# Kernel optimization log

Hardware: AMD Instinct MI355X
Metric: run time of the kernel (lower is better)

Reference implementation:

```python
import jax, jax.numpy as jnp
import numpy as np

B, N, D_IN, D_OUT, H = 8, 1024, 768, 768, 12
D_HEAD = D_OUT // H  # 64; per-head softmax scale is sqrt(D_HEAD)


def setup_inputs() -> dict:
    key = jax.random.key(0)
    kx, kq, kk, kv, kwo, kbo = jax.random.split(key, 6)
    s_in = 1.0 / np.sqrt(D_IN)
    s_out = 1.0 / np.sqrt(D_OUT)
    return {
        "x": jax.random.normal(kx, (B, N, D_IN), dtype=jnp.float32),
        # stacked per-head Linear weights, torch layout [out, in] -> [H, d_head, D_IN]
        "Wq": jax.random.uniform(kq, (H, D_HEAD, D_IN), jnp.float32, -s_in, s_in),
        "Wk": jax.random.uniform(kk, (H, D_HEAD, D_IN), jnp.float32, -s_in, s_in),
        "Wv": jax.random.uniform(kv, (H, D_HEAD, D_IN), jnp.float32, -s_in, s_in),
        "Wo": jax.random.uniform(kwo, (D_OUT, D_OUT), jnp.float32, -s_out, s_out),
        "bo": jax.random.uniform(kbo, (D_OUT,), jnp.float32, -s_out, s_out),
    }


def reference(x, Wq, Wk, Wv, Wo, bo):
    # Per-head projections, batched over heads: [B, H, N, d_head]
    q = jnp.einsum('bnd,hed->bhne', x, Wq)
    k = jnp.einsum('bnd,hed->bhne', x, Wk)
    v = jnp.einsum('bnd,hed->bhne', x, Wv)
    scale = 1.0 / np.sqrt(D_HEAD)
    scores = jnp.einsum('bhie,bhje->bhij', q, k) * scale  # [B, H, N, N]
    att = jax.nn.softmax(scores, axis=-1)
    out = jnp.einsum('bhij,bhje->bhie', att, v)  # [B, H, N, d_head]
    # concat heads along last dim: [B, N, H*d_head]
    out = out.transpose(0, 2, 1, 3).reshape(B, N, D_OUT)
    return out @ Wo.T + bo
```

## Files before the change

### kernel.cpp

```cpp
#include <hip/hip_runtime.h>
#include <hip/hip_bf16.h>


typedef unsigned short u16;
typedef unsigned int u32;
typedef __attribute__((ext_vector_type(8))) short bf8;
typedef __attribute__((ext_vector_type(4))) short bf4;
typedef __attribute__((ext_vector_type(4))) float f4;
typedef __attribute__((ext_vector_type(4))) unsigned short us4;

#define NB 8
#define NSEQ 1024
#define DMODEL 768
#define NHEAD 12
#define DHEAD 64

#define XELEMS   (NB * NSEQ * DMODEL)
#define WELEMS   (DMODEL * DMODEL)

__device__ __forceinline__ float b2f(u16 u) {
  union { unsigned int i; float f; } c; c.i = ((unsigned int)u) << 16; return c.f;
}
__device__ __forceinline__ u16 f2b(float f) {
  union { float f; unsigned int i; } c; c.f = f;
  unsigned int r = c.i + 0x7fffu + ((c.i >> 16) & 1u);
  return (u16)(r >> 16);
}
__device__ __forceinline__ void gl_lds16(const u16* g, u16* l) {
  __builtin_amdgcn_global_load_lds(
      (const __attribute__((address_space(1))) unsigned int*)g,
      (__attribute__((address_space(3))) unsigned int*)l, 16, 0, 0);
}

struct CvtArgs {
  const float* src[5];
  u16* dst[5];
};
#define G0 (XELEMS / 4)
#define GW (WELEMS / 4)
#define GTOT (G0 + 4 * GW)

__global__ __launch_bounds__(256) void cvt_kernel(CvtArgs a) {
  size_t g = (size_t)blockIdx.x * 256 + threadIdx.x;
  if (g >= GTOT) return;
  int t; size_t off;
  if (g < G0) { t = 0; off = g; }
  else { size_t r = g - G0; t = 1 + (int)(r / GW); off = r % GW; }
  f4 v = *(const f4*)(a.src[t] + off * 4);
  us4 o;
  o[0] = f2b(v[0]); o[1] = f2b(v[1]); o[2] = f2b(v[2]); o[3] = f2b(v[3]);
  *(us4*)(a.dst[t] + off * 4) = o;
}

__global__ __launch_bounds__(256, 2) void qkv_gemm(
    const u16* __restrict__ x, const u16* __restrict__ Wq,
    const u16* __restrict__ Wk, const u16* __restrict__ Wv,
    u16* __restrict__ q, u16* __restrict__ k, u16* __restrict__ vt)
{
  __shared__ __align__(16) u16 lA[2][128 * 64];
  __shared__ __align__(16) u16 lB[2][128 * 64];

  const int tid  = threadIdx.x;
  const int lane = tid & 63;
  const int w    = tid >> 6;
  const int wm   = w >> 1;
  const int wn   = w & 1;
  const int col  = lane & 15;
  const int quad = lane >> 4;

  const int bid = blockIdx.x;
  const int xcd = bid & 7;
  const int j   = bid >> 3;
  const int bng = j / 48;
  const int rr  = j % 48;
  const int bm8 = rr / 6;
  const int bn6 = rr % 6;
  const int bm  = xcd * 8 + bm8;
  const int bn  = bng * 6 + bn6;

  const int m0 = bm * 128;
  const int proj = bn / 6;
  const u16* Wsel = (proj == 0) ? Wq : (proj == 1 ? Wk : Wv);
  const int nrem0 = (bn % 6) * 128;

  const int srow8 = lane >> 3;
  const int sg    = (lane & 7) ^ srow8;

  const u16* gA = x    + (size_t)(m0    + w * 32 + srow8) * DMODEL + sg * 8;
  const u16* gB = Wsel + (size_t)(nrem0 + w * 32 + srow8) * DMODEL + sg * 8;

  f4 acc[4][4];
#pragma unroll
  for (int i = 0; i < 4; i++)
#pragma unroll
    for (int jj = 0; jj < 4; jj++) acc[i][jj] = (f4)0.0f;

#define QKV_STAGE(T, BUF)                                                      \
  do {                                                                         \
    const int kk_ = (T) * 64;                                                  \
    _Pragma("unroll")                                                          \
    for (int i_ = 0; i_ < 4; i_++)                                             \
      gl_lds16(gA + (size_t)(i_ * 8) * DMODEL + kk_,                           \
               &lA[BUF][(w * 32 + i_ * 8) * 64]);                              \
    _Pragma("unroll")                                                          \
    for (int i_ = 0; i_ < 4; i_++)                                             \
      gl_lds16(gB + (size_t)(i_ * 8) * DMODEL + kk_,                           \
               &lB[BUF][(w * 32 + i_ * 8) * 64]);                              \
  } while (0)

  QKV_STAGE(0, 0);
  __syncthreads();

  for (int t = 0; t < 12; t++) {
    const int cur = t & 1;
    if (t < 11) QKV_STAGE(t + 1, cur ^ 1);

    bf8 af[4][2], bfr[4][2];
#pragma unroll
    for (int mt = 0; mt < 4; mt++) {
      const int row = wm * 64 + mt * 16 + col;
#pragma unroll
      for (int kt = 0; kt < 2; kt++)
        af[mt][kt] = *(const bf8*)&lA[cur][row * 64 + (((kt * 4 + quad) ^ (row & 7)) << 3)];
    }
#pragma unroll
    for (int nt = 0; nt < 4; nt++) {
      const int row = wn * 64 + nt * 16 + col;
#pragma unroll
      for (int kt = 0; kt < 2; kt++)
        bfr[nt][kt] = *(const bf8*)&lB[cur][row * 64 + (((kt * 4 + quad) ^ (row & 7)) << 3)];
    }

    __builtin_amdgcn_s_setprio(1);
#pragma unroll
    for (int mt = 0; mt < 4; mt++)
#pragma unroll
      for (int nt = 0; nt < 4; nt++)
#pragma unroll
        for (int kt = 0; kt < 2; kt++)
          acc[mt][nt] = __builtin_amdgcn_mfma_f32_16x16x32_bf16(af[mt][kt], bfr[nt][kt], acc[mt][nt], 0, 0, 0);
    __builtin_amdgcn_s_setprio(0);

    __syncthreads();
  }
#undef QKV_STAGE

  const int mw0 = m0 + wm * 64, nw0 = nrem0 + wn * 64;
  if (proj == 2) {
#pragma unroll
    for (int mt = 0; mt < 4; mt++) {
#pragma unroll
      for (int nt = 0; nt < 4; nt++) {
        const int nc = nw0 + nt * 16 + col;
        const int h = nc >> 6, e = nc & 63;
        const int t0 = mw0 + mt * 16 + quad * 4;
        const int b = t0 >> 10, tok0 = t0 & 1023;
        us4 pk;
#pragma unroll
        for (int r = 0; r < 4; r++) pk[r] = f2b(acc[mt][nt][r]);
        *(us4*)(vt + ((size_t)(b * NHEAD + h) * DHEAD + e) * NSEQ + tok0) = pk;
      }
    }
  } else {
    u16* dst = (proj == 0) ? q : k;
#pragma unroll
    for (int mt = 0; mt < 4; mt++) {
#pragma unroll
      for (int nt = 0; nt < 4; nt++) {
        const int nc = nw0 + nt * 16 + col;
        const int h = nc >> 6, e = nc & 63;
#pragma unroll
        for (int r = 0; r < 4; r++) {
          const int t = mw0 + mt * 16 + quad * 4 + r;
          const int b = t >> 10, tok = t & 1023;
          dst[((size_t)(b * NHEAD + h) * NSEQ + tok) * DHEAD + e] = f2b(acc[mt][nt][r]);
        }
      }
    }
  }
}

__global__ __launch_bounds__(256, 3) void attn_kernel(
    const u16* __restrict__ q, const u16* __restrict__ k,
    const u16* __restrict__ vt, u16* __restrict__ attn)
{
  __shared__ __align__(16) u16 ldsK[2][64 * 64];
  __shared__ __align__(16) u16 ldsV[2][64 * 64];
  __shared__ __align__(16) u16 ldsP[4][32][72];

  const int tid  = threadIdx.x;
  const int lane = tid & 63;
  const int w    = tid >> 6;
  const int col  = lane & 15;
  const int quad = lane >> 4;

  const int idx = blockIdx.x;
  const int bh = idx % 96, qc = idx / 96;
  const int b = bh / 12, h = bh % 12;

  const size_t head = ((size_t)b * NHEAD + h) * NSEQ * DHEAD;
  const int q0 = qc * 128 + w * 32;

  const int srow8 = lane >> 3;
  const int sg    = (lane & 7) ^ srow8;

  bf8 onesf;
#pragma unroll
  for (int jj = 0; jj < 8; jj++) onesf[jj] = (short)0x3F80;

  bf8 qf[2][2];
#pragma unroll
  for (int qt = 0; qt < 2; qt++)
#pragma unroll
    for (int kt = 0; kt < 2; kt++) {
      const int row = q0 + qt * 16 + col;
      bf8 t = *(const bf8*)(q + head + (size_t)row * DHEAD + kt * 32 + quad * 8);
#pragma unroll
      for (int jj = 0; jj < 8; jj++) t[jj] = (short)f2b(b2f((u16)t[jj]) * 0.125f);
      qf[qt][kt] = t;
    }

  f4 lacc[2];
  f4 o[2][4];
#pragma unroll
  for (int mt = 0; mt < 2; mt++) {
    lacc[mt] = (f4)0.0f;
#pragma unroll
    for (int et = 0; et < 4; et++) o[mt][et] = (f4)0.0f;
  }

#pragma unroll
  for (int i = 0; i < 2; i++) {
    const int li = w * 2 + i;
    gl_lds16(k  + head + (size_t)(li * 8 + srow8) * DHEAD + sg * 8, &ldsK[0][li * 512]);
    gl_lds16(vt + head + (size_t)(li * 8 + srow8) * NSEQ + sg * 8,  &ldsV[0][li * 512]);
  }

  for (int t = 0; t < NSEQ / 64; t++) {
    const int cur = t & 1;
    __syncthreads();
    if (t < NSEQ / 64 - 1) {
      const int kb2 = (t + 1) * 64;
#pragma unroll
      for (int i = 0; i < 2; i++) {
        const int li = w * 2 + i;
        gl_lds16(k  + head + (size_t)(kb2 + li * 8 + srow8) * DHEAD + sg * 8,
                 &ldsK[cur ^ 1][li * 512]);
        gl_lds16(vt + head + (size_t)(li * 8 + srow8) * NSEQ + kb2 + sg * 8,
                 &ldsV[cur ^ 1][li * 512]);
      }
    }

    f4 st[4][2];
#pragma unroll
    for (int kvt = 0; kvt < 4; kvt++)
#pragma unroll
      for (int qt = 0; qt < 2; qt++) st[kvt][qt] = (f4)0.0f;
#pragma unroll
    for (int kt = 0; kt < 2; kt++) {
      bf8 kf[4];
#pragma unroll
      for (int kvt = 0; kvt < 4; kvt++) {
        const int row = kvt * 16 + col;
        kf[kvt] = *(const bf8*)&ldsK[cur][row * 64 + (((kt * 4 + quad) ^ (col & 7)) << 3)];
      }
      __builtin_amdgcn_s_setprio(1);
#pragma unroll
      for (int kvt = 0; kvt < 4; kvt++)
#pragma unroll
        for (int qt = 0; qt < 2; qt++)
          st[kvt][qt] = __builtin_amdgcn_mfma_f32_16x16x32_bf16(kf[kvt], qf[qt][kt], st[kvt][qt], 0, 0, 0);
      __builtin_amdgcn_s_setprio(0);
    }

#pragma unroll
    for (int kvt = 0; kvt < 4; kvt++)
#pragma unroll
      for (int qt = 0; qt < 2; qt++) {
        const f4 p = st[kvt][qt];
        bf4 pw;
        pw[0] = (short)f2b(__expf(p[0]));
        pw[1] = (short)f2b(__expf(p[1]));
        pw[2] = (short)f2b(__expf(p[2]));
        pw[3] = (short)f2b(__expf(p[3]));
        *(bf4*)&ldsP[w][qt * 16 + col][kvt * 16 + quad * 4] = pw;
      }
    asm volatile("" ::: "memory");

#pragma unroll
    for (int kt2 = 0; kt2 < 2; kt2++) {
      bf8 vf[4];
#pragma unroll
      for (int et = 0; et < 4; et++) {
        const int row = et * 16 + col;
        vf[et] = *(const bf8*)&ldsV[cur][row * 64 + (((kt2 * 4 + quad) ^ (col & 7)) << 3)];
      }
#pragma unroll
      for (int mt = 0; mt < 2; mt++) {
        const bf8 pf = *(const bf8*)&ldsP[w][mt * 16 + col][kt2 * 32 + quad * 8];
        __builtin_amdgcn_s_setprio(1);
        lacc[mt] = __builtin_amdgcn_mfma_f32_16x16x32_bf16(pf, onesf, lacc[mt], 0, 0, 0);
#pragma unroll
        for (int et = 0; et < 4; et++)
          o[mt][et] = __builtin_amdgcn_mfma_f32_16x16x32_bf16(pf, vf[et], o[mt][et], 0, 0, 0);
        __builtin_amdgcn_s_setprio(0);
      }
    }
  }

#pragma unroll
  for (int mt = 0; mt < 2; mt++)
#pragma unroll
    for (int r = 0; r < 4; r++) {
      const float inv = 1.0f / lacc[mt][r];
      const int token = q0 + mt * 16 + quad * 4 + r;
#pragma unroll
      for (int et = 0; et < 4; et++)
        attn[(size_t)(b * NSEQ + token) * DMODEL + h * DHEAD + et * 16 + col] =
            f2b(o[mt][et][r] * inv);
    }
}

__global__ __launch_bounds__(256, 4) void out_gemm(
    const u16* __restrict__ attn, const u16* __restrict__ Wo,
    const float* __restrict__ bo, float* __restrict__ out)
{
  __shared__ __align__(16) u16 lA[2][128 * 32];
  __shared__ __align__(16) u16 lB[2][128 * 32];

  const int tid  = threadIdx.x;
  const int lane = tid & 63;
  const int w    = tid >> 6;
  const int wm   = w >> 1, wn = w & 1;
  const int col  = lane & 15;
  const int quad = lane >> 4;
  const int bm = blockIdx.x;
  const int bn = blockIdx.y;

  const int m0 = bm * 128;
  const int n0 = bn * 128;

  const int srow = lane >> 2;
  const int sg   = (lane & 3) ^ ((srow >> 1) & 3);
  const u16* gA0 = attn + (size_t)(m0 + w * 32 + srow) * DMODEL + sg * 8;
  const u16* gB0 = Wo   + (size_t)(n0 + w * 32 + srow) * DMODEL + sg * 8;

  f4 acc[4][4];
#pragma unroll
  for (int i = 0; i < 4; i++)
#pragma unroll
    for (int jj = 0; jj < 4; jj++) acc[i][jj] = (f4)0.0f;

  gl_lds16(gA0, &lA[0][(w * 32) * 32]);
  gl_lds16(gA0 + (size_t)16 * DMODEL, &lA[0][(w * 32 + 16) * 32]);
  gl_lds16(gB0, &lB[0][(w * 32) * 32]);
  gl_lds16(gB0 + (size_t)16 * DMODEL, &lB[0][(w * 32 + 16) * 32]);

  for (int it = 0; it < 24; it++) {
    const int cur = it & 1;
    __syncthreads();
    if (it < 23) {
      const int kk = (it + 1) * 32;
      gl_lds16(gA0 + kk, &lA[cur ^ 1][(w * 32) * 32]);
      gl_lds16(gA0 + (size_t)16 * DMODEL + kk, &lA[cur ^ 1][(w * 32 + 16) * 32]);
      gl_lds16(gB0 + kk, &lB[cur ^ 1][(w * 32) * 32]);
      gl_lds16(gB0 + (size_t)16 * DMODEL + kk, &lB[cur ^ 1][(w * 32 + 16) * 32]);
    }

    bf8 af[4], bfr[4];
#pragma unroll
    for (int mt = 0; mt < 4; mt++) {
      const int row = wm * 64 + mt * 16 + col;
      af[mt] = *(const bf8*)&lA[cur][row * 32 + ((quad ^ ((row >> 1) & 3)) << 3)];
    }
#pragma unroll
    for (int nt = 0; nt < 4; nt++) {
      const int row = wn * 64 + nt * 16 + col;
      bfr[nt] = *(const bf8*)&lB[cur][row * 32 + ((quad ^ ((row >> 1) & 3)) << 3)];
    }
#pragma unroll
    for (int mt = 0; mt < 4; mt++)
#pragma unroll
      for (int nt = 0; nt < 4; nt++)
        acc[mt][nt] = __builtin_amdgcn_mfma_f32_16x16x32_bf16(af[mt], bfr[nt], acc[mt][nt], 0, 0, 0);
  }

  const int mw0 = m0 + wm * 64, nw0 = n0 + wn * 64;
#pragma unroll
  for (int mt = 0; mt < 4; mt++)
#pragma unroll
    for (int nt = 0; nt < 4; nt++) {
      const int n = nw0 + nt * 16 + col;
      const float bias = bo[n];
#pragma unroll
      for (int r = 0; r < 4; r++) {
        const int row = mw0 + mt * 16 + quad * 4 + r;
        out[(size_t)row * DMODEL + n] = acc[mt][nt][r] + bias;
      }
    }
}

extern "C" void kernel_launch(void* const* d_in, const int* in_sizes, int n_in,
                              void* d_out, int out_size, void* d_ws, size_t ws_size,
                              hipStream_t stream) {
  const float* x  = (const float*)d_in[0];
  const float* Wq = (const float*)d_in[1];
  const float* Wk = (const float*)d_in[2];
  const float* Wv = (const float*)d_in[3];
  const float* Wo = (const float*)d_in[4];
  const float* bo = (const float*)d_in[5];
  float* out = (float*)d_out;

  u16* xb   = (u16*)d_ws;
  u16* wqb  = xb  + XELEMS;
  u16* wkb  = wqb + WELEMS;
  u16* wvb  = wkb + WELEMS;
  u16* wob  = wvb + WELEMS;
  u16* q    = wob + WELEMS;
  u16* k    = q   + XELEMS;
  u16* vt   = k   + XELEMS;
  u16* attn = vt  + XELEMS;

  CvtArgs ca;
  ca.src[0] = x;  ca.src[1] = Wq;  ca.src[2] = Wk;  ca.src[3] = Wv;  ca.src[4] = Wo;
  ca.dst[0] = xb; ca.dst[1] = wqb; ca.dst[2] = wkb; ca.dst[3] = wvb; ca.dst[4] = wob;

  cvt_kernel<<<dim3((GTOT + 255) / 256), 256, 0, stream>>>(ca);
  qkv_gemm<<<dim3(1152), 256, 0, stream>>>(xb, wqb, wkb, wvb, q, k, vt);
  attn_kernel<<<dim3(768), 256, 0, stream>>>(q, k, vt, attn);
  out_gemm<<<dim3(64, 6), 256, 0, stream>>>(attn, wob, bo, out);
}
```

Measured before the change: 185.8 us.

## Fold query scale into QKV epilogue and deepen output GEMM K-tile with XCD swizzle

The 1/sqrt(d_head) scale now multiplies Q in the QKV projection epilogue, so the attention kernel no longer converts and rescales its Q fragments. The output projection GEMM doubles its K tile to 64 with an 8-way XOR swizzle, halving the loop trips and barriers. Its grid becomes 1D with an XCD-aware block remap for L2 locality, and the MFMA block gets raised priority. The larger LDS footprint lowers the occupancy hint from 4 to 2 blocks per CU.

```diff
diff --git a/kernel.cpp b/kernel.cpp
--- a/kernel.cpp
+++ b/kernel.cpp
@@ -163,6 +163,7 @@
     }
   } else {
     u16* dst = (proj == 0) ? q : k;
+    const float scl = (proj == 0) ? 0.125f : 1.0f;
 #pragma unroll
     for (int mt = 0; mt < 4; mt++) {
 #pragma unroll
@@ -173,7 +174,7 @@
         for (int r = 0; r < 4; r++) {
           const int t = mw0 + mt * 16 + quad * 4 + r;
           const int b = t >> 10, tok = t & 1023;
-          dst[((size_t)(b * NHEAD + h) * NSEQ + tok) * DHEAD + e] = f2b(acc[mt][nt][r]);
+          dst[((size_t)(b * NHEAD + h) * NSEQ + tok) * DHEAD + e] = f2b(acc[mt][nt][r] * scl);
         }
       }
     }
@@ -214,10 +215,7 @@
 #pragma unroll
     for (int kt = 0; kt < 2; kt++) {
       const int row = q0 + qt * 16 + col;
-      bf8 t = *(const bf8*)(q + head + (size_t)row * DHEAD + kt * 32 + quad * 8);
-#pragma unroll
-      for (int jj = 0; jj < 8; jj++) t[jj] = (short)f2b(b2f((u16)t[jj]) * 0.125f);
-      qf[qt][kt] = t;
+      qf[qt][kt] = *(const bf8*)(q + head + (size_t)row * DHEAD + kt * 32 + quad * 8);
     }
 
   f4 lacc[2];
@@ -321,29 +319,35 @@
     }
 }
 
-__global__ __launch_bounds__(256, 4) void out_gemm(
+__global__ __launch_bounds__(256, 2) void out_gemm(
     const u16* __restrict__ attn, const u16* __restrict__ Wo,
     const float* __restrict__ bo, float* __restrict__ out)
 {
-  __shared__ __align__(16) u16 lA[2][128 * 32];
-  __shared__ __align__(16) u16 lB[2][128 * 32];
+  __shared__ __align__(16) u16 lA[2][128 * 64];
+  __shared__ __align__(16) u16 lB[2][128 * 64];
 
   const int tid  = threadIdx.x;
   const int lane = tid & 63;
   const int w    = tid >> 6;
-  const int wm   = w >> 1, wn = w & 1;
+  const int wm   = w >> 1;
+  const int wn   = w & 1;
   const int col  = lane & 15;
   const int quad = lane >> 4;
-  const int bm = blockIdx.x;
-  const int bn = blockIdx.y;
+
+  const int bid = blockIdx.x;
+  const int xcd = bid & 7;
+  const int j   = bid >> 3;
+  const int bm  = xcd * 8 + j / 6;
+  const int bn  = j % 6;
 
   const int m0 = bm * 128;
   const int n0 = bn * 128;
 
-  const int srow = lane >> 2;
-  const int sg   = (lane & 3) ^ ((srow >> 1) & 3);
-  const u16* gA0 = attn + (size_t)(m0 + w * 32 + srow) * DMODEL + sg * 8;
-  const u16* gB0 = Wo   + (size_t)(n0 + w * 32 + srow) * DMODEL + sg * 8;
+  const int srow8 = lane >> 3;
+  const int sg    = (lane & 7) ^ srow8;
+
+  const u16* gA = attn + (size_t)(m0 + w * 32 + srow8) * DMODEL + sg * 8;
+  const u16* gB = Wo   + (size_t)(n0 + w * 32 + srow8) * DMODEL + sg * 8;
 
   f4 acc[4][4];
 #pragma unroll
@@ -351,39 +355,55 @@
 #pragma unroll
     for (int jj = 0; jj < 4; jj++) acc[i][jj] = (f4)0.0f;
 
-  gl_lds16(gA0, &lA[0][(w * 32) * 32]);
-  gl_lds16(gA0 + (size_t)16 * DMODEL, &lA[0][(w * 32 + 16) * 32]);
-  gl_lds16(gB0, &lB[0][(w * 32) * 32]);
-  gl_lds16(gB0 + (size_t)16 * DMODEL, &lB[0][(w * 32 + 16) * 32]);
-
-  for (int it = 0; it < 24; it++) {
-    const int cur = it & 1;
-    __syncthreads();
-    if (it < 23) {
-      const int kk = (it + 1) * 32;
-      gl_lds16(gA0 + kk, &lA[cur ^ 1][(w * 32) * 32]);
-      gl_lds16(gA0 + (size_t)16 * DMODEL + kk, &lA[cur ^ 1][(w * 32 + 16) * 32]);
-      gl_lds16(gB0 + kk, &lB[cur ^ 1][(w * 32) * 32]);
-      gl_lds16(gB0 + (size_t)16 * DMODEL + kk, &lB[cur ^ 1][(w * 32 + 16) * 32]);
-    }
-
-    bf8 af[4], bfr[4];
+#define OUT_STAGE(T, BUF)                                                      \
+  do {                                                                         \
+    const int kk_ = (T) * 64;                                                  \
+    _Pragma("unroll")                                                          \
+    for (int i_ = 0; i_ < 4; i_++)                                             \
+      gl_lds16(gA + (size_t)(i_ * 8) * DMODEL + kk_,                           \
+               &lA[BUF][(w * 32 + i_ * 8) * 64]);                              \
+    _Pragma("unroll")                                                          \
+    for (int i_ = 0; i_ < 4; i_++)                                             \
+      gl_lds16(gB + (size_t)(i_ * 8) * DMODEL + kk_,                           \
+               &lB[BUF][(w * 32 + i_ * 8) * 64]);                              \
+  } while (0)
+
+  OUT_STAGE(0, 0);
+  __syncthreads();
+
+  for (int t = 0; t < 12; t++) {
+    const int cur = t & 1;
+    if (t < 11) OUT_STAGE(t + 1, cur ^ 1);
+
+    bf8 af[4][2], bfr[4][2];
 #pragma unroll
     for (int mt = 0; mt < 4; mt++) {
       const int row = wm * 64 + mt * 16 + col;
-      af[mt] = *(const bf8*)&lA[cur][row * 32 + ((quad ^ ((row >> 1) & 3)) << 3)];
+#pragma unroll
+      for (int kt = 0; kt < 2; kt++)
+        af[mt][kt] = *(const bf8*)&lA[cur][row * 64 + (((kt * 4 + quad) ^ (row & 7)) << 3)];
     }
 #pragma unroll
     for (int nt = 0; nt < 4; nt++) {
       const int row = wn * 64 + nt * 16 + col;
-      bfr[nt] = *(const bf8*)&lB[cur][row * 32 + ((quad ^ ((row >> 1) & 3)) << 3)];
-    }
+#pragma unroll
+      for (int kt = 0; kt < 2; kt++)
+        bfr[nt][kt] = *(const bf8*)&lB[cur][row * 64 + (((kt * 4 + quad) ^ (row & 7)) << 3)];
+    }
+
+    __builtin_amdgcn_s_setprio(1);
 #pragma unroll
     for (int mt = 0; mt < 4; mt++)
 #pragma unroll
       for (int nt = 0; nt < 4; nt++)
-        acc[mt][nt] = __builtin_amdgcn_mfma_f32_16x16x32_bf16(af[mt], bfr[nt], acc[mt][nt], 0, 0, 0);
-  }
+#pragma unroll
+        for (int kt = 0; kt < 2; kt++)
+          acc[mt][nt] = __builtin_amdgcn_mfma_f32_16x16x32_bf16(af[mt][kt], bfr[nt][kt], acc[mt][nt], 0, 0, 0);
+    __builtin_amdgcn_s_setprio(0);
+
+    __syncthreads();
+  }
+#undef OUT_STAGE
 
   const int mw0 = m0 + wm * 64, nw0 = n0 + wn * 64;
 #pragma unroll
@@ -428,5 +448,5 @@
   cvt_kernel<<<dim3((GTOT + 255) / 256), 256, 0, stream>>>(ca);
   qkv_gemm<<<dim3(1152), 256, 0, stream>>>(xb, wqb, wkb, wvb, q, k, vt);
   attn_kernel<<<dim3(768), 256, 0, stream>>>(q, k, vt, attn);
-  out_gemm<<<dim3(64, 6), 256, 0, stream>>>(attn, wob, bo, out);
-}
+  out_gemm<<<dim3(384), 256, 0, stream>>>(attn, wob, bo, out);
+}
```

After: 189.0 us. About the same (+1.7%).
